# Performance work log

Hardware: AMD Instinct MI355X
Metric: run time of the kernel (lower is better)

## Reference

```python
import jax, jax.numpy as jnp
import numpy as np

N, T, S = 8192, 512, 32
D = 256          # d_model (h_states feature dim)
H = 256          # query_mlp_hidden_dim
R = 256          # operator rank
RFF = 64
DT = 16
L = 2            # num_query_mlp_layers
NHEAD = 4
HD = H // NHEAD
EPS = 1e-5


def _ln(x, g, b):
    m = jnp.mean(x, axis=-1, keepdims=True)
    v = jnp.mean((x - m) ** 2, axis=-1, keepdims=True)
    return (x - m) * jax.lax.rsqrt(v + EPS) * g + b


def _lin(x, w, b):  # torch Linear: w is [out, in]
    return x @ w.T + b


def rff_encode(x, B):
    p = x @ B
    return jnp.concatenate([jnp.cos(p), jnp.sin(p)], axis=-1)


def setup_inputs() -> dict:
    key = jax.random.key(0)
    ks = iter(jax.random.split(key, 64))
    rn = lambda shape, s=0.05: jax.random.normal(next(ks), shape, jnp.float32) * s
    inp = {}
    inp['xy'] = jax.random.uniform(next(ks), (N, 2), jnp.float32) * 2 * np.pi
    inp['t_q'] = jax.random.uniform(next(ks), (N,), jnp.float32)
    inp['c'] = jax.random.randint(next(ks), (N,), 0, 3)
    inp['h_states'] = rn((T, S, D), 1.0)
    inp['sensor_time'] = jnp.sort(jax.random.uniform(next(ks), (T,), jnp.float32))
    inp['B'] = rn((2, RFF), 1.0)
    q_in = 2 * RFF + DT + 8
    inp['time_w'] = rn((DT, 1)); inp['time_b'] = jnp.zeros((DT,))
    inp['comp_emb'] = rn((3, 8), 0.1)
    inp['trunk_in_w'] = rn((H, q_in)); inp['trunk_in_b'] = jnp.zeros((H,))
    inp['blk_ln_g'] = jnp.ones((L, H)); inp['blk_ln_b'] = jnp.zeros((L, H))
    inp['blk_fc1_w'] = rn((L, H, H)); inp['blk_fc1_b'] = jnp.zeros((L, H))
    inp['blk_fc2_w'] = rn((L, H, H)); inp['blk_fc2_b'] = jnp.zeros((L, H))
    inp['btp_w'] = rn((H, D)); inp['btp_b'] = jnp.zeros((H,))
    inp['bn_g'] = jnp.ones((H,)); inp['bn_b'] = jnp.zeros((H,))
    inp['attn_in_w'] = rn((3 * H, H)); inp['attn_in_b'] = jnp.zeros((3 * H,))
    inp['attn_out_w'] = rn((H, H)); inp['attn_out_b'] = jnp.zeros((H,))
    inp['bc_ln_g'] = jnp.ones((H,)); inp['bc_ln_b'] = jnp.zeros((H,))
    inp['bc_w1'] = rn((H, H)); inp['bc_b1'] = jnp.zeros((H,))
    inp['bc_w2'] = rn((H, H)); inp['bc_b2'] = jnp.zeros((H,))
    inp['trunk_out_w'] = rn((3 * R, H)); inp['trunk_out_b'] = jnp.zeros((3 * R,))
    inp['bproj_w'] = rn((3 * R, H)); inp['bproj_b'] = jnp.zeros((3 * R,))
    inp['log_temp'] = jnp.asarray(np.log(1.0 / np.sqrt(R)), jnp.float32)
    inp['comp_scale'] = jnp.ones((3,)); inp['comp_bias'] = jnp.zeros((3,))
    return inp


def reference(xy, t_q, c, h_states, sensor_time, B, time_w, time_b, comp_emb,
              trunk_in_w, trunk_in_b, blk_ln_g, blk_ln_b, blk_fc1_w, blk_fc1_b,
              blk_fc2_w, blk_fc2_b, btp_w, btp_b, bn_g, bn_b,
              attn_in_w, attn_in_b, attn_out_w, attn_out_b,
              bc_ln_g, bc_ln_b, bc_w1, bc_b1, bc_w2, bc_b2,
              trunk_out_w, trunk_out_b, bproj_w, bproj_b,
              log_temp, comp_scale, comp_bias):
    n = xy.shape[0]
    # time-indexed gather of CfC states
    idx = jnp.searchsorted(sensor_time, t_q, side='right') - 1
    idx = jnp.clip(idx, 0, h_states.shape[0] - 1)
    h_br = h_states[idx]                                   # [N,S,D]
    dt = jnp.maximum(t_q - sensor_time[idx], 0.0)          # [N]
    # trunk path
    rff = rff_encode(xy, B)                                # [N,2*RFF]
    time_e = _lin(dt[:, None], time_w, time_b)             # [N,DT]
    emb_c = comp_emb[c]                                    # [N,8]
    feat = jax.nn.silu(_lin(jnp.concatenate([rff, time_e, emb_c], -1), trunk_in_w, trunk_in_b))
    for i in range(blk_fc1_w.shape[0]):
        y = _ln(feat, blk_ln_g[i], blk_ln_b[i])
        y = jax.nn.silu(_lin(y, blk_fc1_w[i], blk_fc1_b[i]))
        feat = feat + _lin(y, blk_fc2_w[i], blk_fc2_b[i])
    trunk_basis = _lin(feat, trunk_out_w, trunk_out_b).reshape(n, 3, -1)
    # branch path: single-query cross attention over sensor tokens
    tokens = _lin(h_br, btp_w, btp_b)                      # [N,S,H]
    q_in = _ln(feat, bn_g, bn_b)                           # [N,H]
    wq, wk, wv = jnp.split(attn_in_w, 3, axis=0)
    bq, bk, bv = jnp.split(attn_in_b, 3, axis=0)
    q = (q_in @ wq.T + bq).reshape(n, NHEAD, HD)           # [N,h,d]
    k = (tokens @ wk.T + bk).reshape(n, S, NHEAD, HD)
    v = (tokens @ wv.T + bv).reshape(n, S, NHEAD, HD)
    scores = jnp.einsum('nhd,nshd->nhs', q, k) / jnp.sqrt(jnp.asarray(HD, q.dtype))
    attn = jax.nn.softmax(scores, axis=-1)
    ctx = jnp.einsum('nhs,nshd->nhd', attn, v).reshape(n, -1)
    ctx = ctx @ attn_out_w.T + attn_out_b                  # [N,H]
    y = _ln(ctx, bc_ln_g, bc_ln_b)
    y = jax.nn.silu(_lin(y, bc_w1, bc_b1))
    ctx = ctx + _lin(y, bc_w2, bc_b2)
    branch_basis = _lin(ctx, bproj_w, bproj_b).reshape(n, 3, -1)
    # per-component select + rank-contraction fusion
    ar = jnp.arange(n)
    trunk_sel = trunk_basis[ar, c]                         # [N,R]
    branch_sel = branch_basis[ar, c]
    temp = jnp.exp(log_temp).astype(trunk_sel.dtype)
    out = jnp.sum(trunk_sel * branch_sel, axis=1, keepdims=True) * temp
    return out * comp_scale[c][:, None] + comp_bias[c][:, None]
```

## Files before the change

### kernel.cpp

```cpp
#include <hip/hip_runtime.h>
#include <cstdint>
#include <cstddef>

typedef unsigned short u16;
typedef __attribute__((ext_vector_type(8))) short s16x8;
typedef __attribute__((ext_vector_type(4))) float f32x4;

#define NQ   8192
#define TT   512
#define STOK 32
#define LDF  260

__device__ __forceinline__ float b2f(u16 u) {
    return __uint_as_float(((uint32_t)u) << 16);
}
__device__ __forceinline__ u16 f2b(float f) {
    uint32_t x = __float_as_uint(f);
    uint32_t r = (x + 0x7FFFu + ((x >> 16) & 1u)) >> 16;
    return (u16)r;
}
__device__ __forceinline__ float silu_f(float x) { return x / (1.f + expf(-x)); }

__global__ __launch_bounds__(256) void const_kernel(float v, float* __restrict__ out) {
    int i = blockIdx.x * 256 + threadIdx.x;
    if (i < NQ) out[i] = v;
}

__global__ __launch_bounds__(256) void zero_kernel(int* __restrict__ cnt) {
    int i = blockIdx.x * 256 + threadIdx.x;
    if (i < 512) cnt[i] = 0;
}

__global__ __launch_bounds__(256) void feat32_kernel(
    const float* __restrict__ xy, const float* __restrict__ t_q,
    const int* __restrict__ c, const float* __restrict__ st,
    const float* __restrict__ B, const float* __restrict__ tw,
    const float* __restrict__ tb, const float* __restrict__ ce,
    float* __restrict__ FIN, int* __restrict__ IDX) {
    int n = blockIdx.x, t = threadIdx.x;
    float tq = t_q[n];
    int lo = 0, hi = TT;
    while (lo < hi) {
        int mid = (lo + hi) >> 1;
        if (st[mid] <= tq) lo = mid + 1; else hi = mid;
    }
    int idx = lo - 1;
    if (idx < 0) idx = 0;
    float dt = tq - st[idx];
    if (dt < 0.f) dt = 0.f;
    if (t == 0) IDX[n] = idx;
    float x = xy[2 * n], y = xy[2 * n + 1];
    size_t base = (size_t)n * 160;
    if (t < 64) { float p = x * B[t] + y * B[64 + t]; FIN[base + t] = cosf(p); }
    else if (t < 128) { int j = t - 64; float p = x * B[j] + y * B[64 + j]; FIN[base + t] = sinf(p); }
    else if (t < 144) { int j = t - 128; FIN[base + t] = dt * tw[j] + tb[j]; }
    else if (t < 152) { int j = t - 144; FIN[base + t] = ce[c[n] * 8 + j]; }
    else if (t < 160) { FIN[base + t] = 0.f; }
}

__global__ __launch_bounds__(256) void pack_split(
    const float* __restrict__ f1w, const float* __restrict__ f2w,
    const float* __restrict__ aiw, const float* __restrict__ aow,
    const float* __restrict__ w1, const float* __restrict__ w2,
    const float* __restrict__ tiw,
    u16* __restrict__ PH, u16* __restrict__ PL) {
    int i = blockIdx.x * 256 + threadIdx.x;
    if (i >= 565248) return;
    float v;
    size_t pos;
    if (i < 524288) {
        int m = i >> 16, j = i & 65535;
        int col = j >> 8, k = j & 255;
        const float* src;
        switch (m) {
            case 0: src = f1w; break;
            case 1: src = f1w + 65536; break;
            case 2: src = f2w; break;
            case 3: src = f2w + 65536; break;
            case 4: src = aiw; break;
            case 5: src = aow; break;
            case 6: src = w1; break;
            default: src = w2; break;
        }
        v = src[j];
        int ct = col >> 4, m16 = col & 15, k0 = k >> 5, quad = (k >> 3) & 3, jj = k & 7;
        pos = (size_t)m * 65536 + (size_t)(((ct * 8 + k0) * 64 + quad * 16 + m16) * 8 + jj);
    } else {
        int j = i - 524288;
        int col = j / 160, k = j % 160;
        v = (k < 152) ? tiw[col * 152 + k] : 0.f;
        int ct = col >> 4, m16 = col & 15, k0 = k >> 5, quad = (k >> 3) & 3, jj = k & 7;
        pos = 524288 + (size_t)(((ct * 5 + k0) * 64 + quad * 16 + m16) * 8 + jj);
    }
    u16 h = f2b(v);
    PH[pos] = h;
    PL[pos] = f2b(v - b2f(h));
}

__global__ __launch_bounds__(256) void combine_kv32(
    const float* __restrict__ aiw, const float* __restrict__ aib,
    const float* __restrict__ btw, const float* __restrict__ btb,
    u16* __restrict__ WKVb, float* __restrict__ bkv) {
    int kv = blockIdx.x >> 8, m = blockIdx.x & 255;
    int d = threadIdx.x;
    __shared__ float wrow[256];
    wrow[d] = aiw[(size_t)(kv + 1) * 65536 + (size_t)m * 256 + d];
    __syncthreads();
    float acc = 0.f;
#pragma unroll 8
    for (int o = 0; o < 256; o++) acc += wrow[o] * btw[(size_t)o * 256 + d];
    WKVb[(size_t)kv * 65536 + (size_t)m * 256 + d] = f2b(acc);
    float pb = wrow[d] * btb[d];
#pragma unroll
    for (int mm = 32; mm >= 1; mm >>= 1) pb += __shfl_xor(pb, mm);
    __shared__ float red[4];
    if ((d & 63) == 0) red[d >> 6] = pb;
    __syncthreads();
    if (d == 0)
        bkv[kv * 256 + m] = red[0] + red[1] + red[2] + red[3] + aib[(kv + 1) * 256 + m];
}

__global__ __launch_bounds__(256) void mcat_kernel(const float* __restrict__ tow,
                                                   const float* __restrict__ bpw,
                                                   u16* __restrict__ MCATb) {
    const int cc = blockIdx.z;
    const int t0 = blockIdx.x * 16, k0 = blockIdx.y * 16;
    const int lt = threadIdx.x & 15, lj = threadIdx.x >> 4;
    const int ot = threadIdx.x & 15, ok = threadIdx.x >> 4;
    __shared__ float As[16][17], Bs[16][17];
    float acc = 0.f;
    for (int j0 = 0; j0 < 256; j0 += 16) {
        As[lj][lt] = tow[((size_t)cc * 256 + j0 + lj) * 256 + t0 + lt];
        Bs[lj][lt] = bpw[((size_t)cc * 256 + j0 + lj) * 256 + k0 + lt];
        __syncthreads();
#pragma unroll
        for (int jj = 0; jj < 16; jj++) acc += As[jj][ot] * Bs[jj][ok];
        __syncthreads();
    }
    MCATb[((size_t)cc * 256 + t0 + ot) * 256 + k0 + ok] = f2b(acc);
}

__global__ __launch_bounds__(256) void uvs_kernel(
    const float* __restrict__ tow, const float* __restrict__ tob,
    const float* __restrict__ bpw, const float* __restrict__ bpb,
    float* __restrict__ U, float* __restrict__ V, float* __restrict__ S) {
    const int cc = blockIdx.x, t = threadIdx.x;
    float v = 0.f, u = 0.f;
    for (int r = 0; r < 256; r++) {
        v += tow[((size_t)cc * 256 + r) * 256 + t] * bpb[cc * 256 + r];
        u += bpw[((size_t)cc * 256 + r) * 256 + t] * tob[cc * 256 + r];
    }
    V[cc * 256 + t] = v;
    U[cc * 256 + t] = u;
    float sp = tob[cc * 256 + t] * bpb[cc * 256 + t];
#pragma unroll
    for (int m = 32; m >= 1; m >>= 1) sp += __shfl_xor(sp, m);
    __shared__ float red[4];
    if ((t & 63) == 0) red[t >> 6] = sp;
    __syncthreads();
    if (t == 0) S[cc] = red[0] + red[1] + red[2] + red[3];
}

__global__ __launch_bounds__(256) void hist_kernel(const int* __restrict__ IDX,
                                                   int* __restrict__ cnt) {
    int n = blockIdx.x * 256 + threadIdx.x;
    if (n < NQ) atomicAdd(&cnt[IDX[n]], 1);
}
__global__ __launch_bounds__(512) void scan_kernel(const int* __restrict__ cnt,
                                                   int* __restrict__ base,
                                                   int* __restrict__ cur) {
    __shared__ int s[TT];
    int t = threadIdx.x;
    int v = cnt[t];
    s[t] = v;
    __syncthreads();
    for (int off = 1; off < TT; off <<= 1) {
        int add = (t >= off) ? s[t - off] : 0;
        __syncthreads();
        s[t] += add;
        __syncthreads();
    }
    base[t] = s[t] - v;
    cur[t] = s[t] - v;
}
__global__ __launch_bounds__(256) void scat_kernel(const int* __restrict__ IDX,
                                                   int* __restrict__ cur,
                                                   int* __restrict__ perm) {
    int n = blockIdx.x * 256 + threadIdx.x;
    if (n < NQ) {
        int pos = atomicAdd(&cur[IDX[n]], 1);
        perm[pos] = n;
    }
}

template <int ST16, int SEL>
__global__ __launch_bounds__(256) void mgemm_b(
    const float* __restrict__ A, const u16* __restrict__ Wb,
    const float* __restrict__ bias, const int* __restrict__ csel,
    void* __restrict__ Cv, int ldc) {
    __shared__ u16 As[64 * 40];
    __shared__ u16 Ws[64 * 40];
    const int t = threadIdx.x;
    const size_t rb = (size_t)blockIdx.x * 64;
    const size_t cb = (size_t)blockIdx.y * 64;
    const int wave = t >> 6, lane = t & 63;
    const int m16 = lane & 15, quad = lane >> 4;
    const int sr = t >> 2, sk = (t & 3) * 8;
    const float* Ap = A + (rb + sr) * 256 + sk;
    const u16* Wp = Wb + (cb + sr) * 256 + sk;

    f32x4 acc[4] = {};
    for (int k0 = 0; k0 < 256; k0 += 32) {
        float4 a0 = *(const float4*)(Ap + k0);
        float4 a1 = *(const float4*)(Ap + k0 + 4);
        u16 ta[8] = {f2b(a0.x), f2b(a0.y), f2b(a0.z), f2b(a0.w),
                     f2b(a1.x), f2b(a1.y), f2b(a1.z), f2b(a1.w)};
        *(uint4*)&As[sr * 40 + sk] = *(const uint4*)ta;
        *(uint4*)&Ws[sr * 40 + sk] = *(const uint4*)(Wp + k0);
        __syncthreads();
        s16x8 af = *(const s16x8*)&As[(wave * 16 + m16) * 40 + quad * 8];
#pragma unroll
        for (int ct = 0; ct < 4; ct++) {
            s16x8 bf = *(const s16x8*)&Ws[(ct * 16 + m16) * 40 + quad * 8];
            acc[ct] = __builtin_amdgcn_mfma_f32_16x16x32_bf16(af, bf, acc[ct], 0, 0, 0);
        }
        __syncthreads();
    }
#pragma unroll
    for (int ct = 0; ct < 4; ct++) {
        size_t col = cb + ct * 16 + m16;
        float bb = bias ? bias[col] : 0.f;
#pragma unroll
        for (int r = 0; r < 4; r++) {
            size_t row = rb + wave * 16 + quad * 4 + r;
            float x = acc[ct][r] + bb;
            if (SEL) {
                int comp = (int)(col >> 8);
                if (csel[row] == comp)
                    ((float*)Cv)[row * 256 + (col & 255)] = x;
            } else if (ST16) {
                ((u16*)Cv)[row * (size_t)ldc + col] = f2b(x);
            } else {
                ((float*)Cv)[row * (size_t)ldc + col] = x;
            }
        }
    }
}

template <int NK0>
struct WF { s16x8 h[NK0], l[NK0]; };

template <int NK0>
__device__ __forceinline__ void wload(const u16* __restrict__ PH,
                                      const u16* __restrict__ PL, size_t mb,
                                      int wave, int lane, WF<NK0>& w) {
#pragma unroll
    for (int k0 = 0; k0 < NK0; k0++) {
        const size_t wo = mb + ((size_t)(wave * NK0 + k0) * 64 + lane) * 8;
        w.h[k0] = *(const s16x8*)&PH[wo];
        w.l[k0] = *(const s16x8*)&PL[wo];
    }
}

template <int NK0>
__device__ __forceinline__ void cgemm_c(const WF<NK0>& w,
                                        const u16* Ch, const u16* Cl,
                                        int lane, f32x4 (&acc)[2]) {
    acc[0] = (f32x4){0.f, 0.f, 0.f, 0.f};
    acc[1] = (f32x4){0.f, 0.f, 0.f, 0.f};
#pragma unroll
    for (int k0 = 0; k0 < NK0; k0++) {
        s16x8 a0h = *(const s16x8*)&Ch[(k0 * 64 + lane) * 8];
        s16x8 a0l = *(const s16x8*)&Cl[(k0 * 64 + lane) * 8];
        s16x8 a1h = *(const s16x8*)&Ch[((8 + k0) * 64 + lane) * 8];
        s16x8 a1l = *(const s16x8*)&Cl[((8 + k0) * 64 + lane) * 8];
        acc[0] = __builtin_amdgcn_mfma_f32_16x16x32_bf16(a0h, w.h[k0], acc[0], 0, 0, 0);
        acc[0] = __builtin_amdgcn_mfma_f32_16x16x32_bf16(a0l, w.h[k0], acc[0], 0, 0, 0);
        acc[0] = __builtin_amdgcn_mfma_f32_16x16x32_bf16(a0h, w.l[k0], acc[0], 0, 0, 0);
        acc[1] = __builtin_amdgcn_mfma_f32_16x16x32_bf16(a1h, w.h[k0], acc[1], 0, 0, 0);
        acc[1] = __builtin_amdgcn_mfma_f32_16x16x32_bf16(a1l, w.h[k0], acc[1], 0, 0, 0);
        acc[1] = __builtin_amdgcn_mfma_f32_16x16x32_bf16(a1h, w.l[k0], acc[1], 0, 0, 0);
    }
}

__device__ __forceinline__ void ln_split(const float* __restrict__ Fv,
                                         u16* __restrict__ Ch, u16* __restrict__ Cl,
                                         const float* __restrict__ g,
                                         const float* __restrict__ b,
                                         float* __restrict__ mean_s,
                                         float* __restrict__ rstd_s, int t) {
    {
        const int row = t >> 5, q = t & 31;
        const float* fr = Fv + row * LDF;
        float4 v0 = *(const float4*)&fr[q * 4];
        float4 v1 = *(const float4*)&fr[q * 4 + 128];
        float s1 = v0.x + v0.y + v0.z + v0.w + v1.x + v1.y + v1.z + v1.w;
        float s2 = v0.x * v0.x + v0.y * v0.y + v0.z * v0.z + v0.w * v0.w +
                   v1.x * v1.x + v1.y * v1.y + v1.z * v1.z + v1.w * v1.w;
#pragma unroll
        for (int m = 16; m >= 1; m >>= 1) {
            s1 += __shfl_xor(s1, m);
            s2 += __shfl_xor(s2, m);
        }
        if (q == 0) {
            float mean = s1 * (1.f / 256.f);
            mean_s[row] = mean;
            rstd_s[row] = rsqrtf(s2 * (1.f / 256.f) - mean * mean + 1e-5f);
        }
    }
    __syncthreads();
    {
        const int rw = t & 31, qc = t >> 5;
        const float* fr = Fv + rw * LDF + qc * 8;
        float4 v0 = *(const float4*)fr;
        float4 v1 = *(const float4*)(fr + 4);
        const float mean = mean_s[rw], rstd = rstd_s[rw];
        float4 g0 = *(const float4*)&g[qc * 8], g1 = *(const float4*)&g[qc * 8 + 4];
        float4 b0 = *(const float4*)&b[qc * 8], b1 = *(const float4*)&b[qc * 8 + 4];
        float va[8] = {v0.x, v0.y, v0.z, v0.w, v1.x, v1.y, v1.z, v1.w};
        float ga[8] = {g0.x, g0.y, g0.z, g0.w, g1.x, g1.y, g1.z, g1.w};
        float ba[8] = {b0.x, b0.y, b0.z, b0.w, b1.x, b1.y, b1.z, b1.w};
        u16 hv[8], lv[8];
#pragma unroll
        for (int j = 0; j < 8; j++) {
            float x = (va[j] - mean) * rstd * ga[j] + ba[j];
            hv[j] = f2b(x);
            lv[j] = f2b(x - b2f(hv[j]));
        }
        const int c = qc * 8;
        const int off = (((rw >> 4) * 8 + (c >> 5)) * 64 +
                         (((c >> 3) & 3) * 16 + (rw & 15))) * 8;
        *(uint4*)&Ch[off] = *(const uint4*)hv;
        *(uint4*)&Cl[off] = *(const uint4*)lv;
    }
}

__global__ __launch_bounds__(1024) void chain1_kernel(
    const float* __restrict__ FIN, const u16* __restrict__ PH,
    const u16* __restrict__ PL, const float* __restrict__ tib,
    const float* __restrict__ lng, const float* __restrict__ lnb,
    const float* __restrict__ f1b, const float* __restrict__ f2bv,
    const float* __restrict__ bng, const float* __restrict__ bnb,
    const float* __restrict__ aib,
    float* __restrict__ Qb, float* __restrict__ Fg) {
    __shared__ u16 Ch[8192], Cl[8192];
    __shared__ float Fv[32 * LDF];
    __shared__ float mean_s[32], rstd_s[32];
    const int t = threadIdx.x;
    const int wave = t >> 6, lane = t & 63;
    const int m16 = lane & 15, quad = lane >> 4;
    const size_t rb = (size_t)blockIdx.x * 32;
    const int col = wave * 16 + m16;
    f32x4 acc[2];

    {
        const int row = t >> 5, q = t & 31;
        if (q < 20) {
            const float* p = FIN + (rb + row) * 160 + q * 8;
            float4 v0 = *(const float4*)p, v1 = *(const float4*)(p + 4);
            float va[8] = {v0.x, v0.y, v0.z, v0.w, v1.x, v1.y, v1.z, v1.w};
            u16 hv[8], lv[8];
#pragma unroll
            for (int j = 0; j < 8; j++) { hv[j] = f2b(va[j]); lv[j] = f2b(va[j] - b2f(hv[j])); }
            const int c = q * 8;
            const int off = (((row >> 4) * 8 + (c >> 5)) * 64 +
                             (((c >> 3) & 3) * 16 + (row & 15))) * 8;
            *(uint4*)&Ch[off] = *(const uint4*)hv;
            *(uint4*)&Cl[off] = *(const uint4*)lv;
        }
    }

    {
        WF<5> w;
        wload<5>(PH, PL, 524288, wave, lane, w);
        __syncthreads();
        cgemm_c<5>(w, Ch, Cl, lane, acc);
    }
    {
        const float bb = tib[col];
#pragma unroll
        for (int rt = 0; rt < 2; rt++)
#pragma unroll
            for (int r = 0; r < 4; r++)
                Fv[(rt * 16 + quad * 4 + r) * LDF + col] = silu_f(acc[rt][r] + bb);
    }
    __syncthreads();

#pragma unroll
    for (int L = 0; L < 2; L++) {
        ln_split(Fv, Ch, Cl, lng + L * 256, lnb + L * 256, mean_s, rstd_s, t);
        {
            WF<8> w;
            wload<8>(PH, PL, (size_t)L * 65536, wave, lane, w);
            __syncthreads();
            cgemm_c<8>(w, Ch, Cl, lane, acc);
        }
        __syncthreads();
        {
            const float bb = f1b[L * 256 + col];
            const int k0c = col >> 5, qc4 = (col >> 3) & 3, jc = col & 7;
#pragma unroll
            for (int rt = 0; rt < 2; rt++)
#pragma unroll
                for (int r = 0; r < 4; r++) {
                    const int row = rt * 16 + quad * 4 + r;
                    float x = silu_f(acc[rt][r] + bb);
                    const int off = ((rt * 8 + k0c) * 64 + (qc4 * 16 + (row & 15))) * 8 + jc;
                    u16 h = f2b(x);
                    Ch[off] = h;
                    Cl[off] = f2b(x - b2f(h));
                }
        }
        {
            WF<8> w;
            wload<8>(PH, PL, 131072 + (size_t)L * 65536, wave, lane, w);
            __syncthreads();
            cgemm_c<8>(w, Ch, Cl, lane, acc);
        }
        {
            const float bb = f2bv[L * 256 + col];
#pragma unroll
            for (int rt = 0; rt < 2; rt++)
#pragma unroll
                for (int r = 0; r < 4; r++) {
                    const int row = rt * 16 + quad * 4 + r;
                    Fv[row * LDF + col] += acc[rt][r] + bb;
                }
        }
        __syncthreads();
    }

    {
        const int row = t >> 5, q = t & 31;
        const float* fr = Fv + row * LDF + q * 8;
        float4 v0 = *(const float4*)fr, v1 = *(const float4*)(fr + 4);
        float* dst = Fg + (rb + row) * 256 + q * 8;
        *(float4*)dst = v0;
        *(float4*)(dst + 4) = v1;
    }
    ln_split(Fv, Ch, Cl, bng, bnb, mean_s, rstd_s, t);

    {
        WF<8> w;
        wload<8>(PH, PL, 262144, wave, lane, w);
        __syncthreads();
        cgemm_c<8>(w, Ch, Cl, lane, acc);
    }
    {
        const float bb = aib[col];
#pragma unroll
        for (int rt = 0; rt < 2; rt++)
#pragma unroll
            for (int r = 0; r < 4; r++) {
                const int row = rt * 16 + quad * 4 + r;
                Qb[(rb + row) * 256 + col] = acc[rt][r] + bb;
            }
    }
}

__global__ __launch_bounds__(1024) void chain2_kernel(
    const float* __restrict__ CTX, const u16* __restrict__ PH,
    const u16* __restrict__ PL, const float* __restrict__ aob,
    const float* __restrict__ clg, const float* __restrict__ clb,
    const float* __restrict__ b1, const float* __restrict__ b2v,
    float* __restrict__ C2g) {
    __shared__ u16 Ch[8192], Cl[8192];
    __shared__ float Fv[32 * LDF];
    __shared__ float mean_s[32], rstd_s[32];
    const int t = threadIdx.x;
    const int wave = t >> 6, lane = t & 63;
    const int m16 = lane & 15, quad = lane >> 4;
    const size_t rb = (size_t)blockIdx.x * 32;
    const int col = wave * 16 + m16;
    f32x4 acc[2];

    {
        const int row = t >> 5, q = t & 31;
        const float* p = CTX + (rb + row) * 256 + q * 8;
        float4 v0 = *(const float4*)p, v1 = *(const float4*)(p + 4);
        float va[8] = {v0.x, v0.y, v0.z, v0.w, v1.x, v1.y, v1.z, v1.w};
        u16 hv[8], lv[8];
#pragma unroll
        for (int j = 0; j < 8; j++) { hv[j] = f2b(va[j]); lv[j] = f2b(va[j] - b2f(hv[j])); }
        const int c = q * 8;
        const int off = (((row >> 4) * 8 + (c >> 5)) * 64 +
                         (((c >> 3) & 3) * 16 + (row & 15))) * 8;
        *(uint4*)&Ch[off] = *(const uint4*)hv;
        *(uint4*)&Cl[off] = *(const uint4*)lv;
    }

    {
        WF<8> w;
        wload<8>(PH, PL, 327680, wave, lane, w);
        __syncthreads();
        cgemm_c<8>(w, Ch, Cl, lane, acc);
    }
    {
        const float bb = aob[col];
#pragma unroll
        for (int rt = 0; rt < 2; rt++)
#pragma unroll
            for (int r = 0; r < 4; r++)
                Fv[(rt * 16 + quad * 4 + r) * LDF + col] = acc[rt][r] + bb;
    }
    __syncthreads();

    ln_split(Fv, Ch, Cl, clg, clb, mean_s, rstd_s, t);
    {
        WF<8> w;
        wload<8>(PH, PL, 393216, wave, lane, w);
        __syncthreads();
        cgemm_c<8>(w, Ch, Cl, lane, acc);
    }
    __syncthreads();
    {
        const float bb = b1[col];
        const int k0c = col >> 5, qc4 = (col >> 3) & 3, jc = col & 7;
#pragma unroll
        for (int rt = 0; rt < 2; rt++)
#pragma unroll
            for (int r = 0; r < 4; r++) {
                const int row = rt * 16 + quad * 4 + r;
                float x = silu_f(acc[rt][r] + bb);
                const int off = ((rt * 8 + k0c) * 64 + (qc4 * 16 + (row & 15))) * 8 + jc;
                u16 h = f2b(x);
                Ch[off] = h;
                Cl[off] = f2b(x - b2f(h));
            }
    }
    {
        WF<8> w;
        wload<8>(PH, PL, 458752, wave, lane, w);
        __syncthreads();
        cgemm_c<8>(w, Ch, Cl, lane, acc);
    }
    {
        const float bb = b2v[col];
#pragma unroll
        for (int rt = 0; rt < 2; rt++)
#pragma unroll
            for (int r = 0; r < 4; r++) {
                const int row = rt * 16 + quad * 4 + r;
                C2g[(rb + row) * 256 + col] = acc[rt][r] + bb + Fv[row * LDF + col];
            }
    }
}

__global__ __launch_bounds__(256) void attn4_kernel(
    float* __restrict__ QC, const u16* __restrict__ KV,
    const int* __restrict__ idx, const int* __restrict__ perm) {
    __shared__ u16 vsh[STOK * 264];
    __shared__ float qsh[256], attw[4][STOK];
    const int n = perm[blockIdx.x];
    const int t = threadIdx.x;
    qsh[t] = QC[(size_t)n * 256 + t];
    int ii = idx[n];
    ii = ii < 0 ? 0 : (ii > TT - 1 ? TT - 1 : ii);
    const u16* kvb = KV + (size_t)ii * STOK * 512;
#pragma unroll
    for (int i = t; i < 1024; i += 256) {
        int s = i >> 5, dq = (i & 31) * 8;
        *(uint4*)&vsh[s * 264 + dq] = *(const uint4*)&kvb[(size_t)s * 512 + 256 + dq];
    }
    __syncthreads();
    if (t < 128) {
        int h = t >> 5, s = t & 31;
        const u16* kp = kvb + (size_t)s * 512 + h * 64;
        uint4 kv[8];
#pragma unroll
        for (int dq = 0; dq < 8; dq++) kv[dq] = *(const uint4*)(kp + dq * 8);
        float p0 = 0.f, p1 = 0.f;
#pragma unroll
        for (int dq = 0; dq < 8; dq++) {
            const u16* ks = (const u16*)&kv[dq];
            float a0 = 0.f;
#pragma unroll
            for (int j = 0; j < 8; j++) a0 += qsh[h * 64 + dq * 8 + j] * b2f(ks[j]);
            if (dq & 1) p1 += a0; else p0 += a0;
        }
        float sc = (p0 + p1) * 0.125f;
        float mx = sc;
#pragma unroll
        for (int m = 16; m >= 1; m >>= 1) mx = fmaxf(mx, __shfl_xor(mx, m));
        float e = expf(sc - mx);
        float sum = e;
#pragma unroll
        for (int m = 16; m >= 1; m >>= 1) sum += __shfl_xor(sum, m);
        attw[h][s] = e / sum;
    }
    __syncthreads();
    {
        int h = t >> 6;
        float a = 0.f;
#pragma unroll 8
        for (int s = 0; s < STOK; s++) a += attw[h][s] * b2f(vsh[s * 264 + t]);
        QC[(size_t)n * 256 + t] = a;
    }
}

__global__ __launch_bounds__(256) void dot_kernel(
    const float* __restrict__ F, const float* __restrict__ H,
    const float* __restrict__ C2, const int* __restrict__ c,
    const float* __restrict__ U, const float* __restrict__ V,
    const float* __restrict__ S, const float* __restrict__ lt,
    const float* __restrict__ cs, const float* __restrict__ cbv,
    float* __restrict__ out) {
    const int n = blockIdx.x * 4 + (threadIdx.x >> 6);
    const int lane = threadIdx.x & 63;
    const int cc = c[n];
    float4 f4 = *(const float4*)&F[(size_t)n * 256 + lane * 4];
    float4 h4 = *(const float4*)&H[(size_t)n * 256 + lane * 4];
    float4 g4 = *(const float4*)&C2[(size_t)n * 256 + lane * 4];
    float4 v4 = *(const float4*)&V[cc * 256 + lane * 4];
    float4 u4 = *(const float4*)&U[cc * 256 + lane * 4];
    float a = f4.x * (h4.x + v4.x) + f4.y * (h4.y + v4.y) +
              f4.z * (h4.z + v4.z) + f4.w * (h4.w + v4.w) +
              u4.x * g4.x + u4.y * g4.y + u4.z * g4.z + u4.w * g4.w;
#pragma unroll
    for (int m = 32; m >= 1; m >>= 1) a += __shfl_xor(a, m);
    if (lane == 0)
        out[n] = (a + S[cc]) * expf(lt[0]) * cs[cc] + cbv[cc];
}

extern "C" void kernel_launch(void* const* d_in, const int* in_sizes, int n_in,
                              void* d_out, int out_size, void* d_ws, size_t ws_size,
                              hipStream_t stream) {
    float* out = (float*)d_out;
    const dim3 blk(256);

    static const int EXPECT[38] = {
        16384, 8192, 8192, 4194304, 512, 128, 16, 16, 24,
        38912, 256, 512, 512, 131072, 512, 131072, 512,
        65536, 256, 256, 256, 196608, 768, 65536, 256,
        256, 256, 65536, 256, 65536, 256, 196608, 768,
        196608, 768, 1, 3, 3};
    if (n_in != 38) { const_kernel<<<NQ / 256, blk, 0, stream>>>(99.0e6f, out); return; }
    for (int i = 0; i < 38; i++)
        if (in_sizes[i] != EXPECT[i]) {
            const_kernel<<<NQ / 256, blk, 0, stream>>>((100.0f + i) * 1.0e6f, out);
            return;
        }

    const float* xy  = (const float*)d_in[0];
    const float* tq  = (const float*)d_in[1];
    const int*   c   = (const int*)d_in[2];
    const float* hs  = (const float*)d_in[3];
    const float* st  = (const float*)d_in[4];
    const float* Bm  = (const float*)d_in[5];
    const float* tw  = (const float*)d_in[6];
    const float* tbv = (const float*)d_in[7];
    const float* ce  = (const float*)d_in[8];
    const float* tiw = (const float*)d_in[9];
    const float* tib = (const float*)d_in[10];
    const float* lng = (const float*)d_in[11];
    const float* lnb = (const float*)d_in[12];
    const float* f1w = (const float*)d_in[13];
    const float* f1b = (const float*)d_in[14];
    const float* f2w = (const float*)d_in[15];
    const float* f2b_ = (const float*)d_in[16];
    const float* btw = (const float*)d_in[17];
    const float* btb = (const float*)d_in[18];
    const float* bng = (const float*)d_in[19];
    const float* bnb = (const float*)d_in[20];
    const float* aiw = (const float*)d_in[21];
    const float* aib = (const float*)d_in[22];
    const float* aow = (const float*)d_in[23];
    const float* aob = (const float*)d_in[24];
    const float* clg = (const float*)d_in[25];
    const float* clb = (const float*)d_in[26];
    const float* w1  = (const float*)d_in[27];
    const float* b1  = (const float*)d_in[28];
    const float* w2  = (const float*)d_in[29];
    const float* b2  = (const float*)d_in[30];
    const float* tow = (const float*)d_in[31];
    const float* tob = (const float*)d_in[32];
    const float* bpw = (const float*)d_in[33];
    const float* bpb = (const float*)d_in[34];
    const float* lt  = (const float*)d_in[35];
    const float* cs  = (const float*)d_in[36];
    const float* cbv = (const float*)d_in[37];

    char* ws = (char*)d_ws;
    const size_t MB = 1 << 20;
    if (ws_size < 44 * MB) {
        const_kernel<<<NQ / 256, blk, 0, stream>>>(8.0e6f, out);
        return;
    }

    u16*   KV   = (u16*)(ws + 0 * MB);
    char*  S_A  = ws + 16 * MB;
    char*  S_B  = ws + 24 * MB;
    char*  S_C  = ws + 32 * MB;
    char*  misc = ws + 40 * MB;
    float* FIN  = (float*)S_A;
    float* H    = (float*)S_A;
    float* F    = (float*)S_B;
    float* Qb   = (float*)S_C;
    float* C2   = (float*)S_C;
    int*   IDX  = (int*)(misc + 0);
    float* bkv  = (float*)(misc + 32 * 1024);
    float* Ubuf = (float*)(misc + 36 * 1024);
    float* Vbuf = (float*)(misc + 40 * 1024);
    float* Sbuf = (float*)(misc + 44 * 1024);
    int*   CNT  = (int*)(misc + 48 * 1024);
    int*   BASE = (int*)(misc + 52 * 1024);
    int*   CUR  = (int*)(misc + 56 * 1024);
    int*   PERM = (int*)(misc + 60 * 1024);
    u16*   WKVb = (u16*)(misc + 92 * 1024);
    u16*   MCATb= (u16*)(misc + 348 * 1024);
    u16*   PH   = (u16*)(misc + 732 * 1024);
    u16*   PL   = (u16*)(misc + 1836 * 1024);

    const dim3 gKV(TT * STOK / 64, 8);
    const dim3 gSEL(NQ / 64, 12);

    zero_kernel<<<2, blk, 0, stream>>>(CNT);
    pack_split<<<2208, blk, 0, stream>>>(f1w, f2w, aiw, aow, w1, w2, tiw, PH, PL);
    combine_kv32<<<512, blk, 0, stream>>>(aiw, aib, btw, btb, WKVb, bkv);
    mcat_kernel<<<dim3(16, 16, 3), blk, 0, stream>>>(tow, bpw, MCATb);
    uvs_kernel<<<3, blk, 0, stream>>>(tow, tob, bpw, bpb, Ubuf, Vbuf, Sbuf);
    feat32_kernel<<<NQ, blk, 0, stream>>>(xy, tq, c, st, Bm, tw, tbv, ce, FIN, IDX);

    hist_kernel<<<NQ / 256, blk, 0, stream>>>(IDX, CNT);
    scan_kernel<<<1, dim3(512), 0, stream>>>(CNT, BASE, CUR);
    scat_kernel<<<NQ / 256, blk, 0, stream>>>(IDX, CUR, PERM);

    mgemm_b<1, 0><<<gKV, blk, 0, stream>>>(hs, WKVb, bkv, nullptr, KV, 512);

    chain1_kernel<<<NQ / 32, dim3(1024), 0, stream>>>(FIN, PH, PL, tib, lng, lnb,
                                                      f1b, f2b_, bng, bnb, aib, Qb, F);
    attn4_kernel<<<NQ, blk, 0, stream>>>(Qb, KV, IDX, PERM);
    chain2_kernel<<<NQ / 32, dim3(1024), 0, stream>>>(Qb, PH, PL, aob, clg, clb,
                                                      b1, b2, C2);
    mgemm_b<0, 1><<<gSEL, blk, 0, stream>>>(C2, MCATb, nullptr, c, H, 256);
    dot_kernel<<<NQ / 4, blk, 0, stream>>>(F, H, C2, c, Ubuf, Vbuf, Sbuf, lt, cs, cbv, out);
}
```

Measured before the change: 322.1 us.

## Fuse bilinear trunk-branch contraction into chain kernels, drop separate gemm and dot

The per-component bilinear contraction (F·M_c·ctx plus the U and V terms) is moved out of the separate select-GEMM and dot kernels. chain1 now computes G = F·M_c + U for all three components with MFMA, keeping only the row's own component, and stores the F·V+S scalar. chain2 then finishes the dot with its own residual output and writes the final result. MCAT is pre-laid-out into a fragment order that the fused GEMM can load directly. This removes two kernel launches and several N×256 fp32 round trips through global memory. In exchange chain1 does extra MFMA work for all three components, and the low half of the weight split is dropped for M, which lowers precision.

```diff
diff --git a/kernel.cpp b/kernel.cpp
--- a/kernel.cpp
+++ b/kernel.cpp
@@ -137,7 +137,12 @@
         for (int jj = 0; jj < 16; jj++) acc += As[jj][ot] * Bs[jj][ok];
         __syncthreads();
     }
-    MCATb[((size_t)cc * 256 + t0 + ot) * 256 + k0 + ok] = f2b(acc);
+    const int tt = t0 + ot, kk2 = k0 + ok;
+    const int ctk = kk2 >> 4, m16k = kk2 & 15;
+    const int tq0 = tt >> 5, tqd = (tt >> 3) & 3, tj = tt & 7;
+    const size_t pos = (size_t)cc * 65536 +
+                       (size_t)(((ctk * 8 + tq0) * 64 + tqd * 16 + m16k) * 8 + tj);
+    MCATb[pos] = f2b(acc);
 }
 
 __global__ __launch_bounds__(256) void uvs_kernel(
@@ -193,11 +198,10 @@
     }
 }
 
-template <int ST16, int SEL>
+template <int ST16>
 __global__ __launch_bounds__(256) void mgemm_b(
     const float* __restrict__ A, const u16* __restrict__ Wb,
-    const float* __restrict__ bias, const int* __restrict__ csel,
-    void* __restrict__ Cv, int ldc) {
+    const float* __restrict__ bias, void* __restrict__ Cv, int ldc) {
     __shared__ u16 As[64 * 40];
     __shared__ u16 Ws[64 * 40];
     const int t = threadIdx.x;
@@ -234,11 +238,7 @@
         for (int r = 0; r < 4; r++) {
             size_t row = rb + wave * 16 + quad * 4 + r;
             float x = acc[ct][r] + bb;
-            if (SEL) {
-                int comp = (int)(col >> 8);
-                if (csel[row] == comp)
-                    ((float*)Cv)[row * 256 + (col & 255)] = x;
-            } else if (ST16) {
+            if (ST16) {
                 ((u16*)Cv)[row * (size_t)ldc + col] = f2b(x);
             } else {
                 ((float*)Cv)[row * (size_t)ldc + col] = x;
@@ -283,6 +283,38 @@
     }
 }
 
+template <int NK0>
+struct WH { s16x8 h[NK0]; };
+
+template <int NK0>
+__device__ __forceinline__ void wloadH(const u16* __restrict__ M, size_t mb,
+                                       int wave, int lane, WH<NK0>& w) {
+#pragma unroll
+    for (int k0 = 0; k0 < NK0; k0++) {
+        const size_t wo = mb + ((size_t)(wave * NK0 + k0) * 64 + lane) * 8;
+        w.h[k0] = *(const s16x8*)&M[wo];
+    }
+}
+
+template <int NK0>
+__device__ __forceinline__ void cgemm_sA(const WH<NK0>& w,
+                                         const u16* Ch, const u16* Cl,
+                                         int lane, f32x4 (&acc)[2]) {
+    acc[0] = (f32x4){0.f, 0.f, 0.f, 0.f};
+    acc[1] = (f32x4){0.f, 0.f, 0.f, 0.f};
+#pragma unroll
+    for (int k0 = 0; k0 < NK0; k0++) {
+        s16x8 a0h = *(const s16x8*)&Ch[(k0 * 64 + lane) * 8];
+        s16x8 a0l = *(const s16x8*)&Cl[(k0 * 64 + lane) * 8];
+        s16x8 a1h = *(const s16x8*)&Ch[((8 + k0) * 64 + lane) * 8];
+        s16x8 a1l = *(const s16x8*)&Cl[((8 + k0) * 64 + lane) * 8];
+        acc[0] = __builtin_amdgcn_mfma_f32_16x16x32_bf16(a0h, w.h[k0], acc[0], 0, 0, 0);
+        acc[0] = __builtin_amdgcn_mfma_f32_16x16x32_bf16(a0l, w.h[k0], acc[0], 0, 0, 0);
+        acc[1] = __builtin_amdgcn_mfma_f32_16x16x32_bf16(a1h, w.h[k0], acc[1], 0, 0, 0);
+        acc[1] = __builtin_amdgcn_mfma_f32_16x16x32_bf16(a1l, w.h[k0], acc[1], 0, 0, 0);
+    }
+}
+
 __device__ __forceinline__ void ln_split(const float* __restrict__ Fv,
                                          u16* __restrict__ Ch, u16* __restrict__ Cl,
                                          const float* __restrict__ g,
@@ -335,23 +367,49 @@
     }
 }
 
+__device__ __forceinline__ void plain_split(const float* __restrict__ Fv,
+                                            u16* __restrict__ Ch,
+                                            u16* __restrict__ Cl, int t) {
+    const int rw = t & 31, qc = t >> 5;
+    const float* fr = Fv + rw * LDF + qc * 8;
+    float4 v0 = *(const float4*)fr;
+    float4 v1 = *(const float4*)(fr + 4);
+    float va[8] = {v0.x, v0.y, v0.z, v0.w, v1.x, v1.y, v1.z, v1.w};
+    u16 hv[8], lv[8];
+#pragma unroll
+    for (int j = 0; j < 8; j++) {
+        hv[j] = f2b(va[j]);
+        lv[j] = f2b(va[j] - b2f(hv[j]));
+    }
+    const int c = qc * 8;
+    const int off = (((rw >> 4) * 8 + (c >> 5)) * 64 +
+                     (((c >> 3) & 3) * 16 + (rw & 15))) * 8;
+    *(uint4*)&Ch[off] = *(const uint4*)hv;
+    *(uint4*)&Cl[off] = *(const uint4*)lv;
+}
+
 __global__ __launch_bounds__(1024) void chain1_kernel(
     const float* __restrict__ FIN, const u16* __restrict__ PH,
     const u16* __restrict__ PL, const float* __restrict__ tib,
     const float* __restrict__ lng, const float* __restrict__ lnb,
     const float* __restrict__ f1b, const float* __restrict__ f2bv,
     const float* __restrict__ bng, const float* __restrict__ bnb,
-    const float* __restrict__ aib,
-    float* __restrict__ Qb, float* __restrict__ Fg) {
+    const float* __restrict__ aib, const int* __restrict__ cptr,
+    const float* __restrict__ Ub, const float* __restrict__ Vb,
+    const float* __restrict__ Sb, const u16* __restrict__ MC,
+    float* __restrict__ Qb, float* __restrict__ Gp, float* __restrict__ FVS) {
     __shared__ u16 Ch[8192], Cl[8192];
     __shared__ float Fv[32 * LDF];
     __shared__ float mean_s[32], rstd_s[32];
+    __shared__ int cselS[32];
     const int t = threadIdx.x;
     const int wave = t >> 6, lane = t & 63;
     const int m16 = lane & 15, quad = lane >> 4;
     const size_t rb = (size_t)blockIdx.x * 32;
     const int col = wave * 16 + m16;
     f32x4 acc[2];
+
+    if (t < 32) cselS[t] = cptr[rb + t];
 
     {
         const int row = t >> 5, q = t & 31;
@@ -432,14 +490,19 @@
 
     {
         const int row = t >> 5, q = t & 31;
+        const int cc = cselS[row];
         const float* fr = Fv + row * LDF + q * 8;
-        float4 v0 = *(const float4*)fr, v1 = *(const float4*)(fr + 4);
-        float* dst = Fg + (rb + row) * 256 + q * 8;
-        *(float4*)dst = v0;
-        *(float4*)(dst + 4) = v1;
-    }
+        const float* vv = Vb + cc * 256 + q * 8;
+        float4 a0 = *(const float4*)fr, a1 = *(const float4*)(fr + 4);
+        float4 w0 = *(const float4*)vv, w1 = *(const float4*)(vv + 4);
+        float s = a0.x * w0.x + a0.y * w0.y + a0.z * w0.z + a0.w * w0.w +
+                  a1.x * w1.x + a1.y * w1.y + a1.z * w1.z + a1.w * w1.w;
+#pragma unroll
+        for (int m = 16; m >= 1; m >>= 1) s += __shfl_xor(s, m);
+        if (q == 0) FVS[rb + row] = s + Sb[cc];
+    }
+
     ln_split(Fv, Ch, Cl, bng, bnb, mean_s, rstd_s, t);
-
     {
         WF<8> w;
         wload<8>(PH, PL, 262144, wave, lane, w);
@@ -454,6 +517,25 @@
             for (int r = 0; r < 4; r++) {
                 const int row = rt * 16 + quad * 4 + r;
                 Qb[(rb + row) * 256 + col] = acc[rt][r] + bb;
+            }
+    }
+    __syncthreads();
+
+    plain_split(Fv, Ch, Cl, t);
+    __syncthreads();
+#pragma unroll
+    for (int g = 0; g < 3; g++) {
+        WH<8> w;
+        wloadH<8>(MC, (size_t)g * 65536, wave, lane, w);
+        cgemm_sA<8>(w, Ch, Cl, lane, acc);
+        const float uu = Ub[g * 256 + col];
+#pragma unroll
+        for (int rt = 0; rt < 2; rt++)
+#pragma unroll
+            for (int r = 0; r < 4; r++) {
+                const int row = rt * 16 + quad * 4 + r;
+                if (cselS[row] == g)
+                    Gp[(rb + row) * 256 + col] = acc[rt][r] + uu;
             }
     }
 }
@@ -463,16 +545,22 @@
     const u16* __restrict__ PL, const float* __restrict__ aob,
     const float* __restrict__ clg, const float* __restrict__ clb,
     const float* __restrict__ b1, const float* __restrict__ b2v,
-    float* __restrict__ C2g) {
+    const int* __restrict__ cptr, const float* __restrict__ Gp,
+    const float* __restrict__ FVS, const float* __restrict__ lt,
+    const float* __restrict__ cs, const float* __restrict__ cbv,
+    float* __restrict__ out) {
     __shared__ u16 Ch[8192], Cl[8192];
     __shared__ float Fv[32 * LDF];
     __shared__ float mean_s[32], rstd_s[32];
+    __shared__ int cselS[32];
     const int t = threadIdx.x;
     const int wave = t >> 6, lane = t & 63;
     const int m16 = lane & 15, quad = lane >> 4;
     const size_t rb = (size_t)blockIdx.x * 32;
     const int col = wave * 16 + m16;
     f32x4 acc[2];
+
+    if (t < 32) cselS[t] = cptr[rb + t];
 
     {
         const int row = t >> 5, q = t & 31;
@@ -541,8 +629,24 @@
 #pragma unroll
             for (int r = 0; r < 4; r++) {
                 const int row = rt * 16 + quad * 4 + r;
-                C2g[(rb + row) * 256 + col] = acc[rt][r] + bb + Fv[row * LDF + col];
+                Fv[row * LDF + col] += acc[rt][r] + bb;
             }
+    }
+    __syncthreads();
+
+    {
+        const int row = t >> 5, q = t & 31;
+        const int cc = cselS[row];
+        const float* fr = Fv + row * LDF + q * 8;
+        const float* gp = Gp + (rb + row) * 256 + q * 8;
+        float4 a0 = *(const float4*)fr, a1 = *(const float4*)(fr + 4);
+        float4 g0 = *(const float4*)gp, g1 = *(const float4*)(gp + 4);
+        float s = a0.x * g0.x + a0.y * g0.y + a0.z * g0.z + a0.w * g0.w +
+                  a1.x * g1.x + a1.y * g1.y + a1.z * g1.z + a1.w * g1.w;
+#pragma unroll
+        for (int m = 16; m >= 1; m >>= 1) s += __shfl_xor(s, m);
+        if (q == 0)
+            out[rb + row] = (s + FVS[rb + row]) * expf(lt[0]) * cs[cc] + cbv[cc];
     }
 }
 
@@ -596,30 +700,6 @@
         for (int s = 0; s < STOK; s++) a += attw[h][s] * b2f(vsh[s * 264 + t]);
         QC[(size_t)n * 256 + t] = a;
     }
-}
-
-__global__ __launch_bounds__(256) void dot_kernel(
-    const float* __restrict__ F, const float* __restrict__ H,
-    const float* __restrict__ C2, const int* __restrict__ c,
-    const float* __restrict__ U, const float* __restrict__ V,
-    const float* __restrict__ S, const float* __restrict__ lt,
-    const float* __restrict__ cs, const float* __restrict__ cbv,
-    float* __restrict__ out) {
-    const int n = blockIdx.x * 4 + (threadIdx.x >> 6);
-    const int lane = threadIdx.x & 63;
-    const int cc = c[n];
-    float4 f4 = *(const float4*)&F[(size_t)n * 256 + lane * 4];
-    float4 h4 = *(const float4*)&H[(size_t)n * 256 + lane * 4];
-    float4 g4 = *(const float4*)&C2[(size_t)n * 256 + lane * 4];
-    float4 v4 = *(const float4*)&V[cc * 256 + lane * 4];
-    float4 u4 = *(const float4*)&U[cc * 256 + lane * 4];
-    float a = f4.x * (h4.x + v4.x) + f4.y * (h4.y + v4.y) +
-              f4.z * (h4.z + v4.z) + f4.w * (h4.w + v4.w) +
-              u4.x * g4.x + u4.y * g4.y + u4.z * g4.z + u4.w * g4.w;
-#pragma unroll
-    for (int m = 32; m >= 1; m >>= 1) a += __shfl_xor(a, m);
-    if (lane == 0)
-        out[n] = (a + S[cc]) * expf(lt[0]) * cs[cc] + cbv[cc];
 }
 
 extern "C" void kernel_launch(void* const* d_in, const int* in_sizes, int n_in,
@@ -693,10 +773,8 @@
     char*  S_C  = ws + 32 * MB;
     char*  misc = ws + 40 * MB;
     float* FIN  = (float*)S_A;
-    float* H    = (float*)S_A;
-    float* F    = (float*)S_B;
+    float* Gp   = (float*)S_B;
     float* Qb   = (float*)S_C;
-    float* C2   = (float*)S_C;
     int*   IDX  = (int*)(misc + 0);
     float* bkv  = (float*)(misc + 32 * 1024);
     float* Ubuf = (float*)(misc + 36 * 1024);
@@ -710,9 +788,9 @@
     u16*   MCATb= (u16*)(misc + 348 * 1024);
     u16*   PH   = (u16*)(misc + 732 * 1024);
     u16*   PL   = (u16*)(misc + 1836 * 1024);
+    float* FVS  = (float*)(misc + 2940 * 1024);
 
     const dim3 gKV(TT * STOK / 64, 8);
-    const dim3 gSEL(NQ / 64, 12);
 
     zero_kernel<<<2, blk, 0, stream>>>(CNT);
     pack_split<<<2208, blk, 0, stream>>>(f1w, f2w, aiw, aow, w1, w2, tiw, PH, PL);
@@ -725,13 +803,13 @@
     scan_kernel<<<1, dim3(512), 0, stream>>>(CNT, BASE, CUR);
     scat_kernel<<<NQ / 256, blk, 0, stream>>>(IDX, CUR, PERM);
 
-    mgemm_b<1, 0><<<gKV, blk, 0, stream>>>(hs, WKVb, bkv, nullptr, KV, 512);
-
-    chain1_kernel<<<NQ / 32, dim3(1024), 0, stream>>>(FIN, PH, PL, tib, lng, lnb,
-                                                      f1b, f2b_, bng, bnb, aib, Qb, F);
+    mgemm_b<1><<<gKV, blk, 0, stream>>>(hs, WKVb, bkv, KV, 512);
+
+    chain1_kernel<<<NQ / 32, dim3(1024), 0, stream>>>(
+        FIN, PH, PL, tib, lng, lnb, f1b, f2b_, bng, bnb, aib,
+        c, Ubuf, Vbuf, Sbuf, MCATb, Qb, Gp, FVS);
     attn4_kernel<<<NQ, blk, 0, stream>>>(Qb, KV, IDX, PERM);
-    chain2_kernel<<<NQ / 32, dim3(1024), 0, stream>>>(Qb, PH, PL, aob, clg, clb,
-                                                      b1, b2, C2);
-    mgemm_b<0, 1><<<gSEL, blk, 0, stream>>>(C2, MCATb, nullptr, c, H, 256);
-    dot_kernel<<<NQ / 4, blk, 0, stream>>>(F, H, C2, c, Ubuf, Vbuf, Sbuf, lt, cs, cbv, out);
-}
+    chain2_kernel<<<NQ / 32, dim3(1024), 0, stream>>>(
+        Qb, PH, PL, aob, clg, clb, b1, b2,
+        c, Gp, FVS, lt, cs, cbv, out);
+}
```

New measurement: 334.4 us. +3.8%, slower.

## Bucket queries by component and fuse selected GEMM with final dot

Applied to the files above, without the earlier changes.

Queries are grouped by component through a counting sort (histogram, scan, scatter into a second permutation), so each 64-row tile multiplies only its own component's 256-column weight block instead of computing all three and discarding two. The GEMM epilogue then fuses the rank contraction with F and C2 and writes the output directly, which removes the H intermediate buffer and the separate dot kernel. The cost is gathered row loads, a serial block-list build in the scan kernel, and only up to 131 blocks with launch_bounds(256,1) and 16 accumulator tiles, which leaves much of the GPU idle.

```diff
diff --git a/kernel.cpp b/kernel.cpp
--- a/kernel.cpp
+++ b/kernel.cpp
@@ -26,9 +26,11 @@
     if (i < NQ) out[i] = v;
 }
 
-__global__ __launch_bounds__(256) void zero_kernel(int* __restrict__ cnt) {
+__global__ __launch_bounds__(256) void zero_kernel(int* __restrict__ cnt,
+                                                   int* __restrict__ cnt3) {
     int i = blockIdx.x * 256 + threadIdx.x;
     if (i < 512) cnt[i] = 0;
+    if (i >= 512 && i < 515) cnt3[i - 512] = 0;
 }
 
 __global__ __launch_bounds__(256) void feat32_kernel(
@@ -162,13 +164,22 @@
 }
 
 __global__ __launch_bounds__(256) void hist_kernel(const int* __restrict__ IDX,
-                                                   int* __restrict__ cnt) {
+                                                   const int* __restrict__ c,
+                                                   int* __restrict__ cnt,
+                                                   int* __restrict__ cnt3) {
     int n = blockIdx.x * 256 + threadIdx.x;
-    if (n < NQ) atomicAdd(&cnt[IDX[n]], 1);
+    if (n < NQ) {
+        atomicAdd(&cnt[IDX[n]], 1);
+        atomicAdd(&cnt3[c[n]], 1);
+    }
 }
 __global__ __launch_bounds__(512) void scan_kernel(const int* __restrict__ cnt,
                                                    int* __restrict__ base,
-                                                   int* __restrict__ cur) {
+                                                   int* __restrict__ cur,
+                                                   const int* __restrict__ cnt3,
+                                                   int* __restrict__ cur3,
+                                                   int* __restrict__ SEG,
+                                                   int* __restrict__ BLK) {
     __shared__ int s[TT];
     int t = threadIdx.x;
     int v = cnt[t];
@@ -182,22 +193,39 @@
     }
     base[t] = s[t] - v;
     cur[t] = s[t] - v;
+    if (t == 0) {
+        int b0 = cnt3[0], b1 = cnt3[1], b2 = cnt3[2];
+        SEG[0] = 0; SEG[1] = b0; SEG[2] = b0 + b1; SEG[3] = b0 + b1 + b2;
+        cur3[0] = SEG[0]; cur3[1] = SEG[1]; cur3[2] = SEG[2];
+        int bidx = 0;
+        for (int g = 0; g < 3; g++) {
+            int cntg = cnt3[g];
+            int tiles = (cntg + 63) >> 6;
+            for (int tl = 0; tl < tiles; tl++)
+                BLK[bidx++] = (g << 16) | (SEG[g] + tl * 64);
+        }
+        for (; bidx < 131; bidx++) BLK[bidx] = -1;
+    }
 }
 __global__ __launch_bounds__(256) void scat_kernel(const int* __restrict__ IDX,
+                                                   const int* __restrict__ c,
                                                    int* __restrict__ cur,
-                                                   int* __restrict__ perm) {
+                                                   int* __restrict__ cur3,
+                                                   int* __restrict__ perm,
+                                                   int* __restrict__ perm2) {
     int n = blockIdx.x * 256 + threadIdx.x;
     if (n < NQ) {
         int pos = atomicAdd(&cur[IDX[n]], 1);
         perm[pos] = n;
-    }
-}
-
-template <int ST16, int SEL>
+        int pos2 = atomicAdd(&cur3[c[n]], 1);
+        perm2[pos2] = n;
+    }
+}
+
+template <int ST16>
 __global__ __launch_bounds__(256) void mgemm_b(
     const float* __restrict__ A, const u16* __restrict__ Wb,
-    const float* __restrict__ bias, const int* __restrict__ csel,
-    void* __restrict__ Cv, int ldc) {
+    const float* __restrict__ bias, void* __restrict__ Cv, int ldc) {
     __shared__ u16 As[64 * 40];
     __shared__ u16 Ws[64 * 40];
     const int t = threadIdx.x;
@@ -234,15 +262,94 @@
         for (int r = 0; r < 4; r++) {
             size_t row = rb + wave * 16 + quad * 4 + r;
             float x = acc[ct][r] + bb;
-            if (SEL) {
-                int comp = (int)(col >> 8);
-                if (csel[row] == comp)
-                    ((float*)Cv)[row * 256 + (col & 255)] = x;
-            } else if (ST16) {
+            if (ST16) {
                 ((u16*)Cv)[row * (size_t)ldc + col] = f2b(x);
             } else {
                 ((float*)Cv)[row * (size_t)ldc + col] = x;
             }
+        }
+    }
+}
+
+__global__ __launch_bounds__(256, 1) void seldot_kernel(
+    const float* __restrict__ C2, const float* __restrict__ F,
+    const u16* __restrict__ MC, const int* __restrict__ BLK,
+    const int* __restrict__ SEG, const int* __restrict__ perm2,
+    const float* __restrict__ Ub, const float* __restrict__ Vb,
+    const float* __restrict__ Sb, const float* __restrict__ lt,
+    const float* __restrict__ cs, const float* __restrict__ cbv,
+    float* __restrict__ out) {
+    const int bd = BLK[blockIdx.x];
+    if (bd < 0) return;
+    const int g = bd >> 16, rowStart = bd & 0xFFFF;
+    __shared__ u16 As[64 * 40];
+    __shared__ u16 Ws[256 * 40];
+    __shared__ int rowIdx[64];
+    __shared__ float vS[256], uS[256];
+    const int t = threadIdx.x;
+    const int wave = t >> 6, lane = t & 63;
+    const int m16 = lane & 15, quad = lane >> 4;
+    const int sr = t >> 2, sk = (t & 3) * 8;
+    if (t < 64) {
+        int pos = rowStart + t;
+        int segEnd = SEG[g + 1];
+        if (pos >= segEnd) pos = segEnd - 1;
+        rowIdx[t] = perm2[pos];
+    }
+    vS[t] = Vb[g * 256 + t];
+    uS[t] = Ub[g * 256 + t];
+    __syncthreads();
+
+    const float* Ap = C2 + (size_t)rowIdx[sr] * 256 + sk;
+    const u16* Wp = MC + (size_t)g * 65536;
+    f32x4 acc[16];
+#pragma unroll
+    for (int i = 0; i < 16; i++) acc[i] = (f32x4){0.f, 0.f, 0.f, 0.f};
+
+    for (int k0 = 0; k0 < 256; k0 += 32) {
+        float4 a0 = *(const float4*)(Ap + k0);
+        float4 a1 = *(const float4*)(Ap + k0 + 4);
+        u16 ta[8] = {f2b(a0.x), f2b(a0.y), f2b(a0.z), f2b(a0.w),
+                     f2b(a1.x), f2b(a1.y), f2b(a1.z), f2b(a1.w)};
+        *(uint4*)&As[sr * 40 + sk] = *(const uint4*)ta;
+#pragma unroll
+        for (int wr = 0; wr < 4; wr++)
+            *(uint4*)&Ws[(wr * 64 + sr) * 40 + sk] =
+                *(const uint4*)(Wp + (size_t)(wr * 64 + sr) * 256 + k0 + sk);
+        __syncthreads();
+        s16x8 af = *(const s16x8*)&As[(wave * 16 + m16) * 40 + quad * 8];
+#pragma unroll
+        for (int ct = 0; ct < 16; ct++) {
+            s16x8 bf = *(const s16x8*)&Ws[(ct * 16 + m16) * 40 + quad * 8];
+            acc[ct] = __builtin_amdgcn_mfma_f32_16x16x32_bf16(af, bf, acc[ct], 0, 0, 0);
+        }
+        __syncthreads();
+    }
+
+    float tot[4] = {0.f, 0.f, 0.f, 0.f};
+#pragma unroll
+    for (int ct = 0; ct < 16; ct++) {
+        const int col = ct * 16 + m16;
+        const float vv = vS[col], uu = uS[col];
+#pragma unroll
+        for (int r = 0; r < 4; r++) {
+            const int row = wave * 16 + quad * 4 + r;
+            const size_t nb = (size_t)rowIdx[row] * 256 + col;
+            tot[r] += F[nb] * (acc[ct][r] + vv) + uu * C2[nb];
+        }
+    }
+    const float scale = expf(lt[0]) * cs[g];
+    const float sg = Sb[g], cbg = cbv[g];
+#pragma unroll
+    for (int r = 0; r < 4; r++) {
+        float s = tot[r];
+        s += __shfl_xor(s, 1);
+        s += __shfl_xor(s, 2);
+        s += __shfl_xor(s, 4);
+        s += __shfl_xor(s, 8);
+        if (m16 == 0) {
+            const int n = rowIdx[wave * 16 + quad * 4 + r];
+            out[n] = (s + sg) * scale + cbg;
         }
     }
 }
@@ -596,30 +703,6 @@
         for (int s = 0; s < STOK; s++) a += attw[h][s] * b2f(vsh[s * 264 + t]);
         QC[(size_t)n * 256 + t] = a;
     }
-}
-
-__global__ __launch_bounds__(256) void dot_kernel(
-    const float* __restrict__ F, const float* __restrict__ H,
-    const float* __restrict__ C2, const int* __restrict__ c,
-    const float* __restrict__ U, const float* __restrict__ V,
-    const float* __restrict__ S, const float* __restrict__ lt,
-    const float* __restrict__ cs, const float* __restrict__ cbv,
-    float* __restrict__ out) {
-    const int n = blockIdx.x * 4 + (threadIdx.x >> 6);
-    const int lane = threadIdx.x & 63;
-    const int cc = c[n];
-    float4 f4 = *(const float4*)&F[(size_t)n * 256 + lane * 4];
-    float4 h4 = *(const float4*)&H[(size_t)n * 256 + lane * 4];
-    float4 g4 = *(const float4*)&C2[(size_t)n * 256 + lane * 4];
-    float4 v4 = *(const float4*)&V[cc * 256 + lane * 4];
-    float4 u4 = *(const float4*)&U[cc * 256 + lane * 4];
-    float a = f4.x * (h4.x + v4.x) + f4.y * (h4.y + v4.y) +
-              f4.z * (h4.z + v4.z) + f4.w * (h4.w + v4.w) +
-              u4.x * g4.x + u4.y * g4.y + u4.z * g4.z + u4.w * g4.w;
-#pragma unroll
-    for (int m = 32; m >= 1; m >>= 1) a += __shfl_xor(a, m);
-    if (lane == 0)
-        out[n] = (a + S[cc]) * expf(lt[0]) * cs[cc] + cbv[cc];
 }
 
 extern "C" void kernel_launch(void* const* d_in, const int* in_sizes, int n_in,
@@ -693,7 +776,6 @@
     char*  S_C  = ws + 32 * MB;
     char*  misc = ws + 40 * MB;
     float* FIN  = (float*)S_A;
-    float* H    = (float*)S_A;
     float* F    = (float*)S_B;
     float* Qb   = (float*)S_C;
     float* C2   = (float*)S_C;
@@ -710,28 +792,32 @@
     u16*   MCATb= (u16*)(misc + 348 * 1024);
     u16*   PH   = (u16*)(misc + 732 * 1024);
     u16*   PL   = (u16*)(misc + 1836 * 1024);
+    int*   PERM2= (int*)(misc + 2940 * 1024);
+    int*   CNT3 = (int*)(misc + 2972 * 1024);
+    int*   CUR3 = (int*)(misc + 2972 * 1024 + 16);
+    int*   SEG  = (int*)(misc + 2972 * 1024 + 32);
+    int*   BLK  = (int*)(misc + 2972 * 1024 + 64);
 
     const dim3 gKV(TT * STOK / 64, 8);
-    const dim3 gSEL(NQ / 64, 12);
-
-    zero_kernel<<<2, blk, 0, stream>>>(CNT);
+
+    zero_kernel<<<3, blk, 0, stream>>>(CNT, CNT3);
     pack_split<<<2208, blk, 0, stream>>>(f1w, f2w, aiw, aow, w1, w2, tiw, PH, PL);
     combine_kv32<<<512, blk, 0, stream>>>(aiw, aib, btw, btb, WKVb, bkv);
     mcat_kernel<<<dim3(16, 16, 3), blk, 0, stream>>>(tow, bpw, MCATb);
     uvs_kernel<<<3, blk, 0, stream>>>(tow, tob, bpw, bpb, Ubuf, Vbuf, Sbuf);
     feat32_kernel<<<NQ, blk, 0, stream>>>(xy, tq, c, st, Bm, tw, tbv, ce, FIN, IDX);
 
-    hist_kernel<<<NQ / 256, blk, 0, stream>>>(IDX, CNT);
-    scan_kernel<<<1, dim3(512), 0, stream>>>(CNT, BASE, CUR);
-    scat_kernel<<<NQ / 256, blk, 0, stream>>>(IDX, CUR, PERM);
-
-    mgemm_b<1, 0><<<gKV, blk, 0, stream>>>(hs, WKVb, bkv, nullptr, KV, 512);
+    hist_kernel<<<NQ / 256, blk, 0, stream>>>(IDX, c, CNT, CNT3);
+    scan_kernel<<<1, dim3(512), 0, stream>>>(CNT, BASE, CUR, CNT3, CUR3, SEG, BLK);
+    scat_kernel<<<NQ / 256, blk, 0, stream>>>(IDX, c, CUR, CUR3, PERM, PERM2);
+
+    mgemm_b<1><<<gKV, blk, 0, stream>>>(hs, WKVb, bkv, KV, 512);
 
     chain1_kernel<<<NQ / 32, dim3(1024), 0, stream>>>(FIN, PH, PL, tib, lng, lnb,
                                                       f1b, f2b_, bng, bnb, aib, Qb, F);
     attn4_kernel<<<NQ, blk, 0, stream>>>(Qb, KV, IDX, PERM);
     chain2_kernel<<<NQ / 32, dim3(1024), 0, stream>>>(Qb, PH, PL, aob, clg, clb,
                                                       b1, b2, C2);
-    mgemm_b<0, 1><<<gSEL, blk, 0, stream>>>(C2, MCATb, nullptr, c, H, 256);
-    dot_kernel<<<NQ / 4, blk, 0, stream>>>(F, H, C2, c, Ubuf, Vbuf, Sbuf, lt, cs, cbv, out);
-}
+    seldot_kernel<<<131, blk, 0, stream>>>(C2, F, MCATb, BLK, SEG, PERM2,
+                                           Ubuf, Vbuf, Sbuf, lt, cs, cbv, out);
+}
```

Result: slower. 421.8 us (+31.0%).
